# Kernel tuning notes

Hardware: AMD Instinct MI355X
Metric: run time of the kernel (lower is better)

Reference implementation:

```python
import jax, jax.numpy as jnp
import numpy as np

N_NODES = 10000
N_EDGES = 160000
F_IN = 256
HEADS = 4
F_OUT = 256
NEG_SLOPE = 0.2  # PyG GATConv default negative_slope
EPS = 1e-5       # GraphNorm eps


def gat_conv(x, src, dst, W, a_src, a_dst, bias, concat):
    """PyG-style GATConv. x:[N,Fin], W:[Fin,H*C], a_src/a_dst:[H,C], bias:[H*C] or [C].
    src/dst already include self-loops (add_self_loops=True default)."""
    N = x.shape[0]
    H, C = a_src.shape
    h = (x @ W).reshape(N, H, C)                      # per-head projected features
    al_s = jnp.einsum('nhc,hc->nh', h, a_src)          # [N,H]
    al_d = jnp.einsum('nhc,hc->nh', h, a_dst)          # [N,H]
    e = jax.nn.leaky_relu(al_s[src] + al_d[dst], NEG_SLOPE)  # [E,H] raw scores
    # segment softmax over edges grouped by destination node
    m = jax.ops.segment_max(e, dst, num_segments=N)    # [N,H]; every node has a self-loop
    ex = jnp.exp(e - m[dst])
    denom = jax.ops.segment_sum(ex, dst, num_segments=N)
    alpha = ex / denom[dst]                            # [E,H]
    out = jax.ops.segment_sum(h[src] * alpha[:, :, None], dst, num_segments=N)  # [N,H,C]
    out = out.reshape(N, H * C) if concat else out.mean(axis=1)
    return out + bias


def graph_norm(x, w, b, ms):
    """PyG GraphNorm over a single graph: y = w*(x-ms*mean)/sqrt(var+eps)+b."""
    mean = x.mean(axis=0, keepdims=True)
    sh = x - ms * mean
    var = (sh * sh).mean(axis=0, keepdims=True)
    return w * sh / jnp.sqrt(var + EPS) + b


def setup_inputs() -> dict:
    key = jax.random.key(0)
    ks = jax.random.split(key, 12)
    H1 = HEADS * F_IN  # 1024
    s = 0.05
    return {
        'x': jax.random.normal(ks[0], (N_NODES, F_IN), jnp.float32),
        'edge_index': jax.random.randint(ks[1], (2, N_EDGES), 0, N_NODES, jnp.int64),
        'W1': jax.random.normal(ks[2], (F_IN, HEADS * F_IN), jnp.float32) * s,
        'att_src1': jax.random.normal(ks[3], (HEADS, F_IN), jnp.float32) * s,
        'att_dst1': jax.random.normal(ks[4], (HEADS, F_IN), jnp.float32) * s,
        'b1': jnp.zeros((H1,), jnp.float32),
        'gn_w': jnp.ones((H1,), jnp.float32),
        'gn_b': jnp.zeros((H1,), jnp.float32),
        'gn_ms': jnp.ones((H1,), jnp.float32),
        'W2': jax.random.normal(ks[5], (H1, F_OUT), jnp.float32) * s,
        'att_src2': jax.random.normal(ks[6], (1, F_OUT), jnp.float32) * s,
        'att_dst2': jax.random.normal(ks[7], (1, F_OUT), jnp.float32) * s,
        'b2': jnp.zeros((F_OUT,), jnp.float32),
    }


def reference(x, edge_index, W1, att_src1, att_dst1, b1, gn_w, gn_b, gn_ms,
              W2, att_src2, att_dst2, b2):
    N = x.shape[0]
    loop = jnp.arange(N, dtype=edge_index.dtype)
    src = jnp.concatenate([edge_index[0], loop])  # add_self_loops=True
    dst = jnp.concatenate([edge_index[1], loop])
    h = gat_conv(x, src, dst, W1, att_src1, att_dst1, b1, concat=True)   # [N, H*Fin]
    h = graph_norm(h, gn_w, gn_b, gn_ms)
    h = jax.nn.relu(h)
    # F.dropout(training=self.training): eval mode -> identity
    out = gat_conv(h, src, dst, W2, att_src2, att_dst2, b2, concat=False)  # [N, Fout]
    return out
```

## Files before the change

kernel.cpp:

```cpp
#include <hip/hip_runtime.h>
#include <hip/hip_bf16.h>

#define NNODES 10000
#define FIN    256
#define HEADS  4
#define H1DIM  1024
#define FOUT   256
#define NEG    0.2f
#define GNEPS  1e-5f
#define SLOTS  96

typedef unsigned short u16;
typedef __attribute__((ext_vector_type(8))) short bf16x8;
typedef __attribute__((ext_vector_type(4))) float f32x4;

__device__ __forceinline__ float bf2f(u16 u) {
    union { unsigned int i; float f; } v; v.i = ((unsigned int)u) << 16; return v.f;
}
__device__ __forceinline__ u16 f2bf(float f) {
    __hip_bfloat16 h = __float2bfloat16(f);
    union { __hip_bfloat16 h; u16 u; } v; v.h = h; return v.u;
}
__device__ __forceinline__ float lrelu(float v) { return v > 0.f ? v : NEG * v; }

__device__ __forceinline__ void compute_flags(const int* ei, const u16* x,
                                              int& is64, int& isbf)
{
    int or_odd = ei[1] | ei[3] | ei[5] | ei[7] | ei[9] | ei[11];
    is64 = (or_odd == 0) ? 1 : 0;
    int sane = 1;
    for (int i = 0; i < 32; i += 2) {
        u16 w = x[i];
        int e = (w >> 7) & 0xFF;
        if (!(w == 0 || w == 0x8000 || (e >= 100 && e <= 150))) sane = 0;
    }
    isbf = sane;
}

struct CvtDesc { const void* src; float* dst; int n; };
struct CvtTable { CvtDesc d[9]; };

#define T0_N 2500
#define T1_N 256
#define T2_N 256
#define T3_N 9
#define T4_N 665
#define T5_N 512
#define PREP_BLOCKS (T0_N + T1_N + T2_N + T3_N + T4_N + T5_N)

__global__ void prep_kernel(const void* __restrict__ x, const int* __restrict__ ei,
                            const void* __restrict__ W1, const void* __restrict__ W2,
                            const void* __restrict__ as1, const void* __restrict__ ad1,
                            CvtTable smalls,
                            u16* __restrict__ xb, u16* __restrict__ W1t,
                            u16* __restrict__ W2t, float* __restrict__ Pm,
                            int* __restrict__ cursor, int* __restrict__ ssort,
                            int* __restrict__ flag, int* __restrict__ fflag,
                            int NE, int Etot)
{
    __shared__ int sfl[2];
    __shared__ u16 tile[32][33];
    if (threadIdx.x == 0) {
        int is64, isbf;
        compute_flags(ei, (const u16*)x, is64, isbf);
        sfl[0] = is64; sfl[1] = isbf;
        if (blockIdx.x == 0) { flag[0] = is64; fflag[0] = isbf; }
    }
    __syncthreads();
    const int is64 = sfl[0], isbf = sfl[1];
    const int b = blockIdx.x;
    const int tid = threadIdx.x;

    if (b < T0_N) {
        int i4 = (b * 256 + tid) * 4;
        if (i4 >= NNODES * FIN) return;
        if (isbf) {
            *reinterpret_cast<ushort4*>(xb + i4) =
                *reinterpret_cast<const ushort4*>((const u16*)x + i4);
        } else {
            float4 v = *reinterpret_cast<const float4*>((const float*)x + i4);
            ushort4 o; o.x = f2bf(v.x); o.y = f2bf(v.y); o.z = f2bf(v.z); o.w = f2bf(v.w);
            *reinterpret_cast<ushort4*>(xb + i4) = o;
        }
    } else if (b < T0_N + T1_N + T2_N) {
        const int task1 = (b < T0_N + T1_N);
        const int bb = task1 ? (b - T0_N) : (b - T0_N - T1_N);
        const void* W = task1 ? W1 : W2;
        u16* Wt = task1 ? W1t : W2t;
        const int K = task1 ? FIN : H1DIM;
        const int N = task1 ? H1DIM : FOUT;
        int ntiles_n = N >> 5;
        int tk = bb / ntiles_n, tn = bb - tk * ntiles_n;
        if (tk >= (K >> 5)) return;
        int k0 = tk << 5, n0 = tn << 5;
        int r = tid >> 5, cdx = tid & 31;
#pragma unroll
        for (int i = 0; i < 4; i++) {
            int kk = i * 8 + r;
            int srcIdx = (k0 + kk) * N + n0 + cdx;
            u16 v = isbf ? ((const u16*)W)[srcIdx] : f2bf(((const float*)W)[srcIdx]);
            tile[kk][cdx] = v;
        }
        __syncthreads();
#pragma unroll
        for (int i = 0; i < 4; i++) {
            int nn = i * 8 + r;
            Wt[(size_t)(n0 + nn) * K + k0 + cdx] = tile[cdx][nn];
        }
    } else if (b < T0_N + T1_N + T2_N + T3_N) {
        const int bb = b - (T0_N + T1_N + T2_N);
        CvtDesc d = smalls.d[bb];
        int i4 = tid * 4;
        if (i4 >= d.n) return;
        if (isbf) {
            ushort4 u = *reinterpret_cast<const ushort4*>((const u16*)d.src + i4);
            *reinterpret_cast<float4*>(d.dst + i4) =
                make_float4(bf2f(u.x), bf2f(u.y), bf2f(u.z), bf2f(u.w));
        } else {
            *reinterpret_cast<float4*>(d.dst + i4) =
                *reinterpret_cast<const float4*>((const float*)d.src + i4);
        }
    } else if (b < T0_N + T1_N + T2_N + T3_N + T4_N) {
        const int bb = b - (T0_N + T1_N + T2_N + T3_N);
        int e = bb * 256 + tid;
        if (e >= Etot) return;
        int src, dst;
        if (e < NE) {
            src = is64 ? ei[2 * e] : ei[e];
            dst = is64 ? ei[2 * (NE + e)] : ei[NE + e];
        } else {
            src = dst = e - NE;
        }
        if ((unsigned)dst >= NNODES) return;
        if ((unsigned)src >= NNODES) src = 0;
        int idx = atomicAdd(&cursor[dst], 1);
        if (idx < SLOTS) ssort[dst * SLOTS + idx] = src;
    } else {
        const int bb = b - (T0_N + T1_N + T2_N + T3_N + T4_N);
        int wave = tid >> 6, lane = tid & 63;
        int idx = bb * 4 + wave;
        int j = idx >> 8, k = idx & 255;
        int hd = j & 3;
        const void* av = (j < 4) ? as1 : ad1;
        int c = lane * 4;
        int widx = k * H1DIM + hd * FIN + c;
        int aidx = hd * FIN + c;
        float wv0, wv1, wv2, wv3, a0, a1, a2, a3;
        if (isbf) {
            ushort4 wu = *reinterpret_cast<const ushort4*>((const u16*)W1 + widx);
            ushort4 au = *reinterpret_cast<const ushort4*>((const u16*)av + aidx);
            wv0 = bf2f(wu.x); wv1 = bf2f(wu.y); wv2 = bf2f(wu.z); wv3 = bf2f(wu.w);
            a0 = bf2f(au.x); a1 = bf2f(au.y); a2 = bf2f(au.z); a3 = bf2f(au.w);
        } else {
            float4 wf = *reinterpret_cast<const float4*>((const float*)W1 + widx);
            float4 af = *reinterpret_cast<const float4*>((const float*)av + aidx);
            wv0 = wf.x; wv1 = wf.y; wv2 = wf.z; wv3 = wf.w;
            a0 = af.x; a1 = af.y; a2 = af.z; a3 = af.w;
        }
        float acc = wv0 * a0 + wv1 * a1 + wv2 * a2 + wv3 * a3;
#pragma unroll
        for (int off = 32; off > 0; off >>= 1)
            acc += __shfl_xor(acc, off, 64);
        if (lane == 0) Pm[j * FIN + k] = acc;
    }
}

__global__ void alsd1_kernel(const u16* __restrict__ xb, const float* __restrict__ Pm,
                             float* __restrict__ als, float* __restrict__ ald)
{
    int wave = threadIdx.x >> 6, lane = threadIdx.x & 63;
    int n = blockIdx.x * 4 + wave;
    if (n >= NNODES) return;
    ushort4 xv = *reinterpret_cast<const ushort4*>(xb + (size_t)n * FIN + lane * 4);
    float x0 = bf2f(xv.x), x1 = bf2f(xv.y), x2 = bf2f(xv.z), x3 = bf2f(xv.w);
    float r[8];
#pragma unroll
    for (int j = 0; j < 8; j++) {
        float4 p = *reinterpret_cast<const float4*>(Pm + j * FIN + lane * 4);
        r[j] = x0 * p.x + x1 * p.y + x2 * p.z + x3 * p.w;
    }
#pragma unroll
    for (int off = 32; off > 0; off >>= 1)
#pragma unroll
        for (int j = 0; j < 8; j++)
            r[j] += __shfl_xor(r[j], off, 64);
    if (lane == 0) {
        *reinterpret_cast<float4*>(als + n * 4) = make_float4(r[0], r[1], r[2], r[3]);
        *reinterpret_cast<float4*>(ald + n * 4) = make_float4(r[4], r[5], r[6], r[7]);
    }
}

__global__ void agg_x_kernel(const int* __restrict__ cursor, const int* __restrict__ ssort,
                             const float* __restrict__ als, const float* __restrict__ ald,
                             const u16* __restrict__ xb, u16* __restrict__ zbuf)
{
    const int wave = threadIdx.x >> 6, lane = threadIdx.x & 63;
    const int n = blockIdx.x * 4 + wave;
    const bool active = (n < NNODES);
    int e0 = 0, e1 = 0;
    float4 adv = make_float4(0.f, 0.f, 0.f, 0.f);
    if (active) {
        e0 = n * SLOTS;
        e1 = e0 + min(cursor[n], SLOTS);
        adv = *reinterpret_cast<const float4*>(ald + n * 4);
    }

    float m0 = -1e30f, m1 = -1e30f, m2 = -1e30f, m3 = -1e30f;
    for (int e = e0 + lane; e < e1; e += 64) {
        int s = ssort[e];
        float4 av = *reinterpret_cast<const float4*>(als + s * 4);
        m0 = fmaxf(m0, lrelu(av.x + adv.x));
        m1 = fmaxf(m1, lrelu(av.y + adv.y));
        m2 = fmaxf(m2, lrelu(av.z + adv.z));
        m3 = fmaxf(m3, lrelu(av.w + adv.w));
    }
#pragma unroll
    for (int off = 32; off > 0; off >>= 1) {
        m0 = fmaxf(m0, __shfl_xor(m0, off, 64));
        m1 = fmaxf(m1, __shfl_xor(m1, off, 64));
        m2 = fmaxf(m2, __shfl_xor(m2, off, 64));
        m3 = fmaxf(m3, __shfl_xor(m3, off, 64));
    }

    __shared__ float wlds[4][128][4];
    __shared__ int schk[4];
    int myCh = active ? ((e1 - e0 + 127) >> 7) : 0;
    if (lane == 0) schk[wave] = myCh;
    __syncthreads();
    int mc = max(max(schk[0], schk[1]), max(schk[2], schk[3]));

    float d0 = 0, d1 = 0, d2 = 0, d3 = 0;
    float a[4][4];
#pragma unroll
    for (int h = 0; h < 4; h++)
#pragma unroll
        for (int c = 0; c < 4; c++) a[h][c] = 0.f;

    for (int ch = 0; ch < mc; ch++) {
        int cs = e0 + ch * 128;
        int ce = min(cs + 128, e1);
        if (ch < myCh) {
            for (int e = cs + lane; e < ce; e += 64) {
                int s = ssort[e];
                float4 av = *reinterpret_cast<const float4*>(als + s * 4);
                float w0 = __expf(lrelu(av.x + adv.x) - m0);
                float w1 = __expf(lrelu(av.y + adv.y) - m1);
                float w2 = __expf(lrelu(av.z + adv.z) - m2);
                float w3 = __expf(lrelu(av.w + adv.w) - m3);
                *reinterpret_cast<float4*>(&wlds[wave][e - cs][0]) = make_float4(w0, w1, w2, w3);
                d0 += w0; d1 += w1; d2 += w2; d3 += w3;
            }
        }
        __syncthreads();
        if (ch < myCh) {
            int ee = cs;
            for (; ee + 1 < ce; ee += 2) {
                int s0 = ssort[ee];
                int s1 = ssort[ee + 1];
                float4 w0 = *reinterpret_cast<const float4*>(&wlds[wave][ee - cs][0]);
                float4 w1 = *reinterpret_cast<const float4*>(&wlds[wave][ee + 1 - cs][0]);
                ushort4 xv0 = *reinterpret_cast<const ushort4*>(xb + (size_t)s0 * FIN + lane * 4);
                ushort4 xv1 = *reinterpret_cast<const ushort4*>(xb + (size_t)s1 * FIN + lane * 4);
                float p0 = bf2f(xv0.x), p1 = bf2f(xv0.y), p2 = bf2f(xv0.z), p3 = bf2f(xv0.w);
                a[0][0] += w0.x * p0; a[0][1] += w0.x * p1; a[0][2] += w0.x * p2; a[0][3] += w0.x * p3;
                a[1][0] += w0.y * p0; a[1][1] += w0.y * p1; a[1][2] += w0.y * p2; a[1][3] += w0.y * p3;
                a[2][0] += w0.z * p0; a[2][1] += w0.z * p1; a[2][2] += w0.z * p2; a[2][3] += w0.z * p3;
                a[3][0] += w0.w * p0; a[3][1] += w0.w * p1; a[3][2] += w0.w * p2; a[3][3] += w0.w * p3;
                float q0 = bf2f(xv1.x), q1 = bf2f(xv1.y), q2 = bf2f(xv1.z), q3 = bf2f(xv1.w);
                a[0][0] += w1.x * q0; a[0][1] += w1.x * q1; a[0][2] += w1.x * q2; a[0][3] += w1.x * q3;
                a[1][0] += w1.y * q0; a[1][1] += w1.y * q1; a[1][2] += w1.y * q2; a[1][3] += w1.y * q3;
                a[2][0] += w1.z * q0; a[2][1] += w1.z * q1; a[2][2] += w1.z * q2; a[2][3] += w1.z * q3;
                a[3][0] += w1.w * q0; a[3][1] += w1.w * q1; a[3][2] += w1.w * q2; a[3][3] += w1.w * q3;
            }
            if (ee < ce) {
                int s = ssort[ee];
                float4 w = *reinterpret_cast<const float4*>(&wlds[wave][ee - cs][0]);
                ushort4 xv = *reinterpret_cast<const ushort4*>(xb + (size_t)s * FIN + lane * 4);
                float x0 = bf2f(xv.x), x1 = bf2f(xv.y), x2 = bf2f(xv.z), x3 = bf2f(xv.w);
                a[0][0] += w.x * x0; a[0][1] += w.x * x1; a[0][2] += w.x * x2; a[0][3] += w.x * x3;
                a[1][0] += w.y * x0; a[1][1] += w.y * x1; a[1][2] += w.y * x2; a[1][3] += w.y * x3;
                a[2][0] += w.z * x0; a[2][1] += w.z * x1; a[2][2] += w.z * x2; a[2][3] += w.z * x3;
                a[3][0] += w.w * x0; a[3][1] += w.w * x1; a[3][2] += w.w * x2; a[3][3] += w.w * x3;
            }
        }
        __syncthreads();
    }
    if (!active) return;
#pragma unroll
    for (int off = 32; off > 0; off >>= 1) {
        d0 += __shfl_xor(d0, off, 64);
        d1 += __shfl_xor(d1, off, 64);
        d2 += __shfl_xor(d2, off, 64);
        d3 += __shfl_xor(d3, off, 64);
    }
    float invs[4];
    invs[0] = d0 > 0.f ? 1.f / d0 : 0.f;
    invs[1] = d1 > 0.f ? 1.f / d1 : 0.f;
    invs[2] = d2 > 0.f ? 1.f / d2 : 0.f;
    invs[3] = d3 > 0.f ? 1.f / d3 : 0.f;
#pragma unroll
    for (int h = 0; h < 4; h++) {
        ushort4 o;
        o.x = f2bf(a[h][0] * invs[h]);
        o.y = f2bf(a[h][1] * invs[h]);
        o.z = f2bf(a[h][2] * invs[h]);
        o.w = f2bf(a[h][3] * invs[h]);
        *reinterpret_cast<ushort4*>(zbuf + (size_t)h * NNODES * FIN + (size_t)n * FIN + lane * 4) = o;
    }
}

#define LDS_STRIDE 40
#define KCHUNK2 1024
template<int BM, int BN, int MINW, bool NORM_A, bool BIAS, bool STATS, bool AL2>
__global__ void __launch_bounds__(256, MINW)
mfma_gemm(const u16* __restrict__ A, const u16* __restrict__ Bt,
          u16* __restrict__ C,
          const float* __restrict__ bias,
          float* __restrict__ gsum, float* __restrict__ gsum2,
          const float* __restrict__ gnw, const float* __restrict__ gnb,
          const float* __restrict__ gnms,
          const float* __restrict__ a2s, const float* __restrict__ a2d,
          float* __restrict__ al2s, float* __restrict__ al2d,
          int M, int K, int ldc, long aZ, long bZ, int cZ, int nbx)
{
    constexpr int MI = BM / 32;
    constexpr int NI = BN / 32;
    constexpr int NLOADS = (BM * 4 + BN * 4) / 256;
    __shared__ u16 Alds[BM * LDS_STRIDE];
    __shared__ u16 Blds[BN * LDS_STRIDE];
    __shared__ float sc_lds[NORM_A ? KCHUNK2 : 1];
    __shared__ float sh_lds[NORM_A ? KCHUNK2 : 1];

    int bid = blockIdx.x;
    {
        int nwg = gridDim.x;
        int q = nwg >> 3, r = nwg & 7;
        int xcd = bid & 7, l = bid >> 3;
        bid = (xcd < r ? xcd * (q + 1) : r * (q + 1) + (xcd - r) * q) + l;
    }
    const int bx = bid % nbx;
    const int by = bid / nbx;

    const u16* Az = A + (long)blockIdx.z * aZ;
    const u16* Bz = Bt + (long)blockIdx.z * bZ;

    const int tid  = threadIdx.x;
    const int lane = tid & 63;
    const int wave = tid >> 6;
    const int wm = wave >> 1, wn = wave & 1;
    const int l15 = lane & 15, quad = lane >> 4;
    const int n0 = bx * BN;
    const int m0 = by * BM;

    if (NORM_A) {
        const float invN = 1.0f / (float)NNODES;
        for (int i = tid; i < K; i += 256) {
            float mean = gsum[i] * invN;
            float ex2  = gsum2[i] * invN;
            float msv  = gnms[i];
            float var  = ex2 - 2.f * msv * mean * mean + msv * msv * mean * mean;
            float sc   = gnw[i] * rsqrtf(fmaxf(var, 0.f) + GNEPS);
            sc_lds[i] = sc;
            sh_lds[i] = gnb[i] - sc * msv * mean;
        }
        __syncthreads();
    }

    int lrow[NLOADS], lcol[NLOADS];
    bool lIsA[NLOADS];
#pragma unroll
    for (int i = 0; i < NLOADS; i++) {
        int g = i * 256 + tid;
        lIsA[i] = g < BM * 4;
        int gg = lIsA[i] ? g : g - BM * 4;
        lrow[i] = gg >> 2;
        lcol[i] = (gg & 3) * 8;
    }
    uint4 pre[NLOADS];

    auto issue = [&](int kt) {
#pragma unroll
        for (int i = 0; i < NLOADS; i++) {
            if (lIsA[i]) {
                int gr = m0 + lrow[i];
                pre[i] = (gr < M)
                    ? *reinterpret_cast<const uint4*>(Az + (size_t)gr * K + kt + lcol[i])
                    : make_uint4(0u, 0u, 0u, 0u);
            } else {
                pre[i] = *reinterpret_cast<const uint4*>(Bz + (size_t)(n0 + lrow[i]) * K + kt + lcol[i]);
            }
        }
    };
    auto commit = [&](int kt) {
#pragma unroll
        for (int i = 0; i < NLOADS; i++) {
            uint4 v = pre[i];
            if (lIsA[i]) {
                if (NORM_A) {
                    int kr = kt + lcol[i];
                    float4 s0 = *reinterpret_cast<const float4*>(&sc_lds[kr]);
                    float4 s1 = *reinterpret_cast<const float4*>(&sc_lds[kr + 4]);
                    float4 h0 = *reinterpret_cast<const float4*>(&sh_lds[kr]);
                    float4 h1 = *reinterpret_cast<const float4*>(&sh_lds[kr + 4]);
                    float sc[8] = {s0.x, s0.y, s0.z, s0.w, s1.x, s1.y, s1.z, s1.w};
                    float sh[8] = {h0.x, h0.y, h0.z, h0.w, h1.x, h1.y, h1.z, h1.w};
                    u16* pv = reinterpret_cast<u16*>(&v);
#pragma unroll
                    for (int j = 0; j < 8; j++)
                        pv[j] = f2bf(fmaxf(0.f, bf2f(pv[j]) * sc[j] + sh[j]));
                }
                *reinterpret_cast<uint4*>(&Alds[lrow[i] * LDS_STRIDE + lcol[i]]) = v;
            } else {
                *reinterpret_cast<uint4*>(&Blds[lrow[i] * LDS_STRIDE + lcol[i]]) = v;
            }
        }
    };

    f32x4 acc[MI][NI];
#pragma unroll
    for (int i = 0; i < MI; i++)
#pragma unroll
        for (int j = 0; j < NI; j++) acc[i][j] = (f32x4){0.f, 0.f, 0.f, 0.f};

    issue(0);
    for (int kt = 0; kt < K; kt += 32) {
        commit(kt);
        __syncthreads();
        if (kt + 32 < K) issue(kt + 32);

        bf16x8 a_frag[MI], b_frag[NI];
#pragma unroll
        for (int mi = 0; mi < MI; mi++)
            a_frag[mi] = *reinterpret_cast<const bf16x8*>(
                &Alds[(wm * (BM / 2) + mi * 16 + l15) * LDS_STRIDE + quad * 8]);
#pragma unroll
        for (int ni = 0; ni < NI; ni++)
            b_frag[ni] = *reinterpret_cast<const bf16x8*>(
                &Blds[(wn * (BN / 2) + ni * 16 + l15) * LDS_STRIDE + quad * 8]);
#pragma unroll
        for (int mi = 0; mi < MI; mi++)
#pragma unroll
            for (int ni = 0; ni < NI; ni++)
                acc[mi][ni] = __builtin_amdgcn_mfma_f32_16x16x32_bf16(
                    a_frag[mi], b_frag[ni], acc[mi][ni], 0, 0, 0);
        __syncthreads();
    }

    float sacc[NI], qacc[NI];
#pragma unroll
    for (int ni = 0; ni < NI; ni++) { sacc[ni] = 0.f; qacc[ni] = 0.f; }

#pragma unroll
    for (int mi = 0; mi < MI; mi++) {
#pragma unroll
        for (int r = 0; r < 4; r++) {
            int row = m0 + wm * (BM / 2) + mi * 16 + quad * 4 + r;
            if (row >= M) continue;
            float ps = 0.f, pd = 0.f;
#pragma unroll
            for (int ni = 0; ni < NI; ni++) {
                int col = n0 + wn * (BN / 2) + ni * 16 + l15;
                float v = acc[mi][ni][r];
                if (BIAS) v += bias[blockIdx.z * cZ + col];
                if (STATS) { sacc[ni] += v; qacc[ni] += v * v; }
                if (AL2) { ps += v * a2s[col]; pd += v * a2d[col]; }
                C[(size_t)row * ldc + blockIdx.z * cZ + col] = f2bf(v);
            }
            if (AL2) {
                ps += __shfl_xor(ps, 1, 64); pd += __shfl_xor(pd, 1, 64);
                ps += __shfl_xor(ps, 2, 64); pd += __shfl_xor(pd, 2, 64);
                ps += __shfl_xor(ps, 4, 64); pd += __shfl_xor(pd, 4, 64);
                ps += __shfl_xor(ps, 8, 64); pd += __shfl_xor(pd, 8, 64);
                if (l15 == 0) {
                    atomicAdd(&al2s[row], ps);
                    atomicAdd(&al2d[row], pd);
                }
            }
        }
    }
    if (STATS) {
#pragma unroll
        for (int ni = 0; ni < NI; ni++) {
            float s = sacc[ni], q = qacc[ni];
            s += __shfl_xor(s, 16, 64); q += __shfl_xor(q, 16, 64);
            s += __shfl_xor(s, 32, 64); q += __shfl_xor(q, 32, 64);
            if (quad == 0) {
                int ch = blockIdx.z * cZ + n0 + wn * (BN / 2) + ni * 16 + l15;
                atomicAdd(&gsum[ch], s);
                atomicAdd(&gsum2[ch], q);
            }
        }
    }
}

__global__ void agg2_kernel(const int* __restrict__ cursor, const int* __restrict__ ssort,
                            const float* __restrict__ als, const float* __restrict__ ald,
                            const u16* __restrict__ h2, const float* __restrict__ b2,
                            const int* __restrict__ fflag, void* __restrict__ outv)
{
    const int wave = threadIdx.x >> 6, lane = threadIdx.x & 63;
    const int n = blockIdx.x * 4 + wave;
    const bool active = (n < NNODES);
    int e0 = 0, e1 = 0;
    float adv = 0.f;
    if (active) {
        e0 = n * SLOTS;
        e1 = e0 + min(cursor[n], SLOTS);
        adv = ald[n];
    }

    float m = -1e30f;
    for (int e = e0 + lane; e < e1; e += 64) {
        int s = ssort[e];
        m = fmaxf(m, lrelu(als[s] + adv));
    }
#pragma unroll
    for (int off = 32; off > 0; off >>= 1)
        m = fmaxf(m, __shfl_xor(m, off, 64));

    __shared__ float wlds[4][128];
    __shared__ int schk[4];
    int myCh = active ? ((e1 - e0 + 127) >> 7) : 0;
    if (lane == 0) schk[wave] = myCh;
    __syncthreads();
    int mc = max(max(schk[0], schk[1]), max(schk[2], schk[3]));

    float d = 0.f, a0 = 0.f, a1 = 0.f, a2 = 0.f, a3 = 0.f;
    for (int ch = 0; ch < mc; ch++) {
        int cs = e0 + ch * 128;
        int ce = min(cs + 128, e1);
        if (ch < myCh) {
            for (int e = cs + lane; e < ce; e += 64) {
                int s = ssort[e];
                float w = __expf(lrelu(als[s] + adv) - m);
                wlds[wave][e - cs] = w;
                d += w;
            }
        }
        __syncthreads();
        if (ch < myCh) {
            int ee = cs;
            for (; ee + 1 < ce; ee += 2) {
                int s0 = ssort[ee];
                int s1 = ssort[ee + 1];
                float w0 = wlds[wave][ee - cs];
                float w1 = wlds[wave][ee + 1 - cs];
                ushort4 hv0 = *reinterpret_cast<const ushort4*>(h2 + (size_t)s0 * FOUT + lane * 4);
                ushort4 hv1 = *reinterpret_cast<const ushort4*>(h2 + (size_t)s1 * FOUT + lane * 4);
                a0 += w0 * bf2f(hv0.x); a1 += w0 * bf2f(hv0.y);
                a2 += w0 * bf2f(hv0.z); a3 += w0 * bf2f(hv0.w);
                a0 += w1 * bf2f(hv1.x); a1 += w1 * bf2f(hv1.y);
                a2 += w1 * bf2f(hv1.z); a3 += w1 * bf2f(hv1.w);
            }
            if (ee < ce) {
                int s = ssort[ee];
                float w = wlds[wave][ee - cs];
                ushort4 hv = *reinterpret_cast<const ushort4*>(h2 + (size_t)s * FOUT + lane * 4);
                a0 += w * bf2f(hv.x); a1 += w * bf2f(hv.y);
                a2 += w * bf2f(hv.z); a3 += w * bf2f(hv.w);
            }
        }
        __syncthreads();
    }
    if (!active) return;
#pragma unroll
    for (int off = 32; off > 0; off >>= 1)
        d += __shfl_xor(d, off, 64);
    float inv = d > 0.f ? 1.f / d : 0.f;
    int c = lane * 4;
    float4 bv = *reinterpret_cast<const float4*>(b2 + c);
    float r0 = a0 * inv + bv.x;
    float r1 = a1 * inv + bv.y;
    float r2 = a2 * inv + bv.z;
    float r3 = a3 * inv + bv.w;
    if (fflag[0]) {
        ushort4 o;
        o.x = f2bf(r0); o.y = f2bf(r1); o.z = f2bf(r2); o.w = f2bf(r3);
        *reinterpret_cast<ushort4*>((u16*)outv + (size_t)n * FOUT + c) = o;
    } else {
        *reinterpret_cast<float4*>((float*)outv + (size_t)n * FOUT + c) =
            make_float4(r0, r1, r2, r3);
    }
}

extern "C" void kernel_launch(void* const* d_in, const int* in_sizes, int n_in,
                              void* d_out, int out_size, void* d_ws, size_t ws_size,
                              hipStream_t stream)
{
    const void* x    = d_in[0];
    const int*  ei   = (const int*)d_in[1];
    const void* W1   = d_in[2];
    const void* as1  = d_in[3];
    const void* ad1  = d_in[4];
    const void* b1   = d_in[5];
    const void* gnw  = d_in[6];
    const void* gnb  = d_in[7];
    const void* gnms = d_in[8];
    const void* W2   = d_in[9];
    const void* as2  = d_in[10];
    const void* ad2  = d_in[11];
    const void* b2   = d_in[12];

    const int NE   = in_sizes[1] / 2;
    const int Etot = NE + NNODES;

    char* w = (char*)d_ws;
    size_t off = 0;
    auto carve = [&](size_t bytes) -> char* {
        char* p = w + off;
        off = (off + bytes + 255) & ~(size_t)255;
        return p;
    };
    int*   cursor = (int*)carve((size_t)NNODES * 4);
    float* gsum   = (float*)carve(1024 * 4);
    float* gsum2  = (float*)carve(1024 * 4);
    float* al2s   = (float*)carve((size_t)NNODES * 4);
    float* al2d   = (float*)carve((size_t)NNODES * 4);
    size_t zero_bytes = off;
    int*   flag   = (int*)carve(256);
    int*   fflag  = (int*)carve(256);
    int*   ssort  = (int*)carve((size_t)NNODES * SLOTS * 4);
    u16*   zbuf   = (u16*)carve((size_t)HEADS * NNODES * FIN * 2);
    u16*   out1b  = (u16*)carve((size_t)NNODES * H1DIM * 2);
    float* al1s   = (float*)carve((size_t)NNODES * HEADS * 4);
    float* al1d   = (float*)carve((size_t)NNODES * HEADS * 4);
    u16*   xb     = (u16*)carve((size_t)NNODES * FIN * 2);
    u16*   W1t    = (u16*)carve((size_t)H1DIM * FIN * 2);
    u16*   W2t    = (u16*)carve((size_t)FOUT * H1DIM * 2);
    float* Pm     = (float*)carve(8 * FIN * 4);
    float* b1f    = (float*)carve(1024 * 4);
    float* gnwf   = (float*)carve(1024 * 4);
    float* gnbf   = (float*)carve(1024 * 4);
    float* gnmsf  = (float*)carve(1024 * 4);
    float* as2f   = (float*)carve(256 * 4);
    float* ad2f   = (float*)carve(256 * 4);
    float* b2f    = (float*)carve(256 * 4);
    float* as1f   = (float*)carve(1024 * 4);
    float* ad1f   = (float*)carve(1024 * 4);
    (void)ws_size;

    u16* h2b = xb;

    hipMemsetAsync(d_ws, 0, zero_bytes, stream);

    {
        CvtTable tab;
        tab.d[0] = { b1,   b1f,   H1DIM };
        tab.d[1] = { gnw,  gnwf,  H1DIM };
        tab.d[2] = { gnb,  gnbf,  H1DIM };
        tab.d[3] = { gnms, gnmsf, H1DIM };
        tab.d[4] = { as2,  as2f,  FOUT };
        tab.d[5] = { ad2,  ad2f,  FOUT };
        tab.d[6] = { b2,   b2f,   FOUT };
        tab.d[7] = { as1,  as1f,  H1DIM };
        tab.d[8] = { ad1,  ad1f,  H1DIM };
        prep_kernel<<<PREP_BLOCKS, 256, 0, stream>>>(x, ei, W1, W2, as1, ad1, tab,
                                                     xb, W1t, W2t, Pm, cursor, ssort,
                                                     flag, fflag, NE, Etot);
    }
    alsd1_kernel<<<2500, 256, 0, stream>>>(xb, Pm, al1s, al1d);
    agg_x_kernel<<<2500, 256, 0, stream>>>(cursor, ssort, al1s, al1d, xb, zbuf);
    {
        const int nbx = FIN / 128;
        const int nby = (NNODES + 63) / 64;
        dim3 grd(nbx * nby, 1, HEADS);
        mfma_gemm<64, 128, 4, false, true, true, false><<<grd, 256, 0, stream>>>(
            zbuf, W1t, out1b, b1f, gsum, gsum2, nullptr, nullptr, nullptr,
            nullptr, nullptr, nullptr, nullptr,
            NNODES, FIN, H1DIM, (long)NNODES * FIN, (long)FIN * FIN, FIN, nbx);
    }
    {
        const int nbx = FOUT / 64;
        const int nby = (NNODES + 63) / 64;
        dim3 grd(nbx * nby, 1, 1);
        mfma_gemm<64, 64, 4, true, false, false, true><<<grd, 256, 0, stream>>>(
            out1b, W2t, h2b, nullptr, gsum, gsum2, gnwf, gnbf, gnmsf,
            as2f, ad2f, al2s, al2d,
            NNODES, H1DIM, FOUT, 0L, 0L, 0, nbx);
    }
    agg2_kernel<<<2500, 256, 0, stream>>>(cursor, ssort, al2s, al2d, h2b, b2f, fflag, d_out);
}
```

Measured before the change: 215.2 us.

## Deepen GEMM K-step to 64 with two register prefetch stages and smaller first tile

```diff
diff --git a/kernel.cpp b/kernel.cpp
--- a/kernel.cpp
+++ b/kernel.cpp
@@ -310,7 +310,6 @@
 }
 
 #define LDS_STRIDE 40
-#define KCHUNK2 1024
 template<int BM, int BN, int MINW, bool NORM_A, bool BIAS, bool STATS, bool AL2>
 __global__ void __launch_bounds__(256, MINW)
 mfma_gemm(const u16* __restrict__ A, const u16* __restrict__ Bt,
@@ -325,11 +324,11 @@
 {
     constexpr int MI = BM / 32;
     constexpr int NI = BN / 32;
-    constexpr int NLOADS = (BM * 4 + BN * 4) / 256;
-    __shared__ u16 Alds[BM * LDS_STRIDE];
-    __shared__ u16 Blds[BN * LDS_STRIDE];
-    __shared__ float sc_lds[NORM_A ? KCHUNK2 : 1];
-    __shared__ float sh_lds[NORM_A ? KCHUNK2 : 1];
+    constexpr int NLOADS = (BM * 8 + BN * 8) / 256;
+    __shared__ u16 Alds[2 * BM * LDS_STRIDE];
+    __shared__ u16 Blds[2 * BN * LDS_STRIDE];
+    __shared__ float sc_lds[NORM_A ? H1DIM : 1];
+    __shared__ float sh_lds[NORM_A ? H1DIM : 1];
 
     int bid = blockIdx.x;
     {
@@ -366,38 +365,40 @@
         __syncthreads();
     }
 
-    int lrow[NLOADS], lcol[NLOADS];
+    int lrow[NLOADS], lk8[NLOADS];
     bool lIsA[NLOADS];
 #pragma unroll
     for (int i = 0; i < NLOADS; i++) {
         int g = i * 256 + tid;
-        lIsA[i] = g < BM * 4;
-        int gg = lIsA[i] ? g : g - BM * 4;
-        lrow[i] = gg >> 2;
-        lcol[i] = (gg & 3) * 8;
-    }
-    uint4 pre[NLOADS];
-
-    auto issue = [&](int kt) {
+        lIsA[i] = g < BM * 8;
+        int gg = lIsA[i] ? g : g - BM * 8;
+        lrow[i] = gg >> 3;
+        lk8[i]  = gg & 7;
+    }
+
+    auto issue = [&](uint4* pre, int kt) {
 #pragma unroll
         for (int i = 0; i < NLOADS; i++) {
+            int kc = kt + lk8[i] * 8;
             if (lIsA[i]) {
                 int gr = m0 + lrow[i];
                 pre[i] = (gr < M)
-                    ? *reinterpret_cast<const uint4*>(Az + (size_t)gr * K + kt + lcol[i])
+                    ? *reinterpret_cast<const uint4*>(Az + (size_t)gr * K + kc)
                     : make_uint4(0u, 0u, 0u, 0u);
             } else {
-                pre[i] = *reinterpret_cast<const uint4*>(Bz + (size_t)(n0 + lrow[i]) * K + kt + lcol[i]);
+                pre[i] = *reinterpret_cast<const uint4*>(Bz + (size_t)(n0 + lrow[i]) * K + kc);
             }
         }
     };
-    auto commit = [&](int kt) {
+    auto commit = [&](uint4* pre, int kt) {
 #pragma unroll
         for (int i = 0; i < NLOADS; i++) {
             uint4 v = pre[i];
+            int half = lk8[i] >> 2;
+            int kk = (lk8[i] & 3) * 8;
             if (lIsA[i]) {
                 if (NORM_A) {
-                    int kr = kt + lcol[i];
+                    int kr = kt + lk8[i] * 8;
                     float4 s0 = *reinterpret_cast<const float4*>(&sc_lds[kr]);
                     float4 s1 = *reinterpret_cast<const float4*>(&sc_lds[kr + 4]);
                     float4 h0 = *reinterpret_cast<const float4*>(&sh_lds[kr]);
@@ -409,9 +410,9 @@
                     for (int j = 0; j < 8; j++)
                         pv[j] = f2bf(fmaxf(0.f, bf2f(pv[j]) * sc[j] + sh[j]));
                 }
-                *reinterpret_cast<uint4*>(&Alds[lrow[i] * LDS_STRIDE + lcol[i]]) = v;
+                *reinterpret_cast<uint4*>(&Alds[(half * BM + lrow[i]) * LDS_STRIDE + kk]) = v;
             } else {
-                *reinterpret_cast<uint4*>(&Blds[lrow[i] * LDS_STRIDE + lcol[i]]) = v;
+                *reinterpret_cast<uint4*>(&Blds[(half * BN + lrow[i]) * LDS_STRIDE + kk]) = v;
             }
         }
     };
@@ -422,27 +423,40 @@
 #pragma unroll
         for (int j = 0; j < NI; j++) acc[i][j] = (f32x4){0.f, 0.f, 0.f, 0.f};
 
-    issue(0);
-    for (int kt = 0; kt < K; kt += 32) {
-        commit(kt);
-        __syncthreads();
-        if (kt + 32 < K) issue(kt + 32);
-
-        bf16x8 a_frag[MI], b_frag[NI];
-#pragma unroll
-        for (int mi = 0; mi < MI; mi++)
-            a_frag[mi] = *reinterpret_cast<const bf16x8*>(
-                &Alds[(wm * (BM / 2) + mi * 16 + l15) * LDS_STRIDE + quad * 8]);
-#pragma unroll
-        for (int ni = 0; ni < NI; ni++)
-            b_frag[ni] = *reinterpret_cast<const bf16x8*>(
-                &Blds[(wn * (BN / 2) + ni * 16 + l15) * LDS_STRIDE + quad * 8]);
-#pragma unroll
-        for (int mi = 0; mi < MI; mi++)
+    auto compute = [&]() {
+#pragma unroll
+        for (int h = 0; h < 2; h++) {
+            bf16x8 a_frag[MI], b_frag[NI];
+#pragma unroll
+            for (int mi = 0; mi < MI; mi++)
+                a_frag[mi] = *reinterpret_cast<const bf16x8*>(
+                    &Alds[(h * BM + wm * (BM / 2) + mi * 16 + l15) * LDS_STRIDE + quad * 8]);
 #pragma unroll
             for (int ni = 0; ni < NI; ni++)
-                acc[mi][ni] = __builtin_amdgcn_mfma_f32_16x16x32_bf16(
-                    a_frag[mi], b_frag[ni], acc[mi][ni], 0, 0, 0);
+                b_frag[ni] = *reinterpret_cast<const bf16x8*>(
+                    &Blds[(h * BN + wn * (BN / 2) + ni * 16 + l15) * LDS_STRIDE + quad * 8]);
+#pragma unroll
+            for (int mi = 0; mi < MI; mi++)
+#pragma unroll
+                for (int ni = 0; ni < NI; ni++)
+                    acc[mi][ni] = __builtin_amdgcn_mfma_f32_16x16x32_bf16(
+                        a_frag[mi], b_frag[ni], acc[mi][ni], 0, 0, 0);
+        }
+    };
+
+    uint4 p0[NLOADS], p1[NLOADS];
+    issue(p0, 0);
+    issue(p1, 64);
+    for (int kt = 0; kt < K; kt += 128) {
+        commit(p0, kt);
+        __syncthreads();
+        if (kt + 128 < K) issue(p0, kt + 128);
+        compute();
+        __syncthreads();
+        commit(p1, kt + 64);
+        __syncthreads();
+        if (kt + 192 < K) issue(p1, kt + 192);
+        compute();
         __syncthreads();
     }
 
@@ -661,10 +675,10 @@
     alsd1_kernel<<<2500, 256, 0, stream>>>(xb, Pm, al1s, al1d);
     agg_x_kernel<<<2500, 256, 0, stream>>>(cursor, ssort, al1s, al1d, xb, zbuf);
     {
-        const int nbx = FIN / 128;
+        const int nbx = FIN / 64;
         const int nby = (NNODES + 63) / 64;
         dim3 grd(nbx * nby, 1, HEADS);
-        mfma_gemm<64, 128, 4, false, true, true, false><<<grd, 256, 0, stream>>>(
+        mfma_gemm<64, 64, 4, false, true, true, false><<<grd, 256, 0, stream>>>(
             zbuf, W1t, out1b, b1f, gsum, gsum2, nullptr, nullptr, nullptr,
             nullptr, nullptr, nullptr, nullptr,
             NNODES, FIN, H1DIM, (long)NNODES * FIN, (long)FIN * FIN, FIN, nbx);
```

Result: slower. 224.6 us (+4.4%).
